# Optimization experiments

Hardware: AMD Instinct MI355X
Metric: run time of the kernel (lower is better)

## Reference

```python
import jax, jax.numpy as jnp
import numpy as np

K = 16          # top-k per pooled row
EPS = 1e-12     # tf.nn.l2_normalize epsilon


def setup_inputs() -> dict:
    key = jax.random.key(0)
    x = jax.random.normal(key, (16, 256, 128, 128), dtype=jnp.float32)
    return {"x": x}


def reference(x) -> tuple:
    # x: [B, C, H, W]; last_n_dims = 2 -> pool the trailing H*W axis.
    B, C, H, W = x.shape
    flat = x.reshape(B, C, H * W)                       # [B, C, HW]
    # tf.nn.l2_normalize(axis=-1): x / sqrt(max(sum(x^2), eps))
    sq = jnp.sum(flat * flat, axis=-1, keepdims=True)
    normed = flat * jax.lax.rsqrt(jnp.maximum(sq, EPS))  # [B, C, HW]
    top_k_value, top_k_idx = jax.lax.top_k(normed, K)    # [B, C, K]
    # decode flat indices into (h, w) coordinates (div/mod loop in original)
    h = top_k_idx // W
    w = top_k_idx % W
    coors = jnp.stack([h, w], axis=-1).astype(jnp.int32)  # [B, C, K, 2]
    return top_k_value, coors
```

## Files before the change

### kernel.cpp

```cpp
#include <hip/hip_runtime.h>


#define KSEL 16
#define HW   16384
#define QSZ  4096
#define WDIM 128
#define CAP  1024
#define CAPQ 256
#define T0   2.5f
#define NROWS 4096
#define NQ   (NROWS * 4)
#define VALS_TOTAL (NROWS * KSEL)

typedef float floatx4 __attribute__((ext_vector_type(4)));


__global__ __launch_bounds__(256) void k1_stream(const float* __restrict__ x,
                                                 float* __restrict__ qsum,
                                                 unsigned* __restrict__ qcnt,
                                                 unsigned long long* __restrict__ qcand) {
    const int b    = blockIdx.x;
    const int row  = b >> 2;
    const int q    = b & 3;
    const int t    = threadIdx.x;
    const int lane = t & 63;

    __shared__ unsigned long long s_cand[CAPQ];
    __shared__ unsigned s_cnt;
    __shared__ float s_part[4];

    if (t == 0) s_cnt = 0;
    __syncthreads();

    const floatx4* p = (const floatx4*)(x + (size_t)row * HW + q * QSZ);

    floatx4 buf[4];
    #pragma unroll
    for (int k = 0; k < 4; ++k)
        buf[k] = __builtin_nontemporal_load(&p[k * 256 + t]);

    float sumsq = 0.0f;
    #pragma unroll
    for (int k = 0; k < 4; ++k) {
        sumsq = fmaf(buf[k].x, buf[k].x, sumsq);
        sumsq = fmaf(buf[k].y, buf[k].y, sumsq);
        sumsq = fmaf(buf[k].z, buf[k].z, sumsq);
        sumsq = fmaf(buf[k].w, buf[k].w, sumsq);
    }

    unsigned msk = 0;
    #pragma unroll
    for (int k = 0; k < 4; ++k) {
        msk |= (buf[k].x > T0) ? (1u << (4 * k + 0)) : 0u;
        msk |= (buf[k].y > T0) ? (1u << (4 * k + 1)) : 0u;
        msk |= (buf[k].z > T0) ? (1u << (4 * k + 2)) : 0u;
        msk |= (buf[k].w > T0) ? (1u << (4 * k + 3)) : 0u;
    }
    unsigned base = 0;
    if (msk) base = atomicAdd(&s_cnt, (unsigned)__popc(msk));
    if (msk) {
        #pragma unroll
        for (int k = 0; k < 4; ++k) {
            #pragma unroll
            for (int c = 0; c < 4; ++c) {
                float v = (c == 0) ? buf[k].x : (c == 1) ? buf[k].y
                        : (c == 2) ? buf[k].z : buf[k].w;
                if (v > T0) {
                    if (base < CAPQ) {
                        unsigned u  = __float_as_uint(v);
                        unsigned mm = u ^ (((unsigned)((int)u >> 31)) | 0x80000000u);
                        int idx = q * QSZ + (k * 256 + t) * 4 + c;
                        s_cand[base] = ((unsigned long long)mm << 32) |
                                       (unsigned)(16383 - idx);
                    }
                    base++;
                }
            }
        }
    }

    #pragma unroll
    for (int off = 32; off > 0; off >>= 1)
        sumsq += __shfl_down(sumsq, off, 64);
    if (lane == 0) s_part[t >> 6] = sumsq;
    __syncthreads();

    unsigned cnt = s_cnt;
    unsigned wr = cnt < CAPQ ? cnt : CAPQ;
    for (unsigned i = t; i < wr; i += 256)
        qcand[(size_t)b * CAPQ + i] = s_cand[i];
    if (t == 0) {
        qcnt[b] = cnt;
        qsum[b] = s_part[0] + s_part[1] + s_part[2] + s_part[3];
    }
}

__global__ __launch_bounds__(256) void k2_select(const float* __restrict__ x,
                                                 const float* __restrict__ qsum,
                                                 const unsigned* __restrict__ qcnt,
                                                 const unsigned long long* __restrict__ qcand,
                                                 float* __restrict__ out) {
    const int row = blockIdx.x;
    const int t   = threadIdx.x;

    __shared__ unsigned long long s_cand[CAP];
    __shared__ unsigned s_qc[4];
    __shared__ float s_qs[4];
    __shared__ unsigned s_cnt;
    __shared__ float s_scale;

    if (t < 4) {
        s_qc[t] = qcnt[row * 4 + t];
        s_qs[t] = qsum[row * 4 + t];
    }
    __syncthreads();

    const unsigned c0 = s_qc[0], c1 = s_qc[1], c2 = s_qc[2], c3 = s_qc[3];
    if (t == 0)
        s_scale = 1.0f / sqrtf(fmaxf(s_qs[0] + s_qs[1] + s_qs[2] + s_qs[3], 1e-12f));
    const bool ovf = (c0 > CAPQ) | (c1 > CAPQ) | (c2 > CAPQ) | (c3 > CAPQ);
    const unsigned tot = c0 + c1 + c2 + c3;

    unsigned cnt;
    if (!ovf && tot >= KSEL && tot <= CAP) {
        const unsigned off[4] = {0u, c0, c0 + c1, c0 + c1 + c2};
        const unsigned cc[4]  = {c0, c1, c2, c3};
        #pragma unroll
        for (int q = 0; q < 4; ++q)
            for (unsigned i = t; i < cc[q]; i += 256)
                s_cand[off[q] + i] = qcand[(size_t)(row * 4 + q) * CAPQ + i];
        cnt = tot;
        __syncthreads();
    } else {
        const float* xr = x + (size_t)row * HW;
        float T = T0, lo = -3.0e38f, hi = 3.0e38f;
        cnt = 0;
        for (int it = 0; it < 32; ++it) {
            __syncthreads();
            if (t == 0) s_cnt = 0;
            __syncthreads();
            for (int i = t; i < HW; i += 256) {
                float v = xr[i];
                if (v > T) {
                    unsigned slot = atomicAdd(&s_cnt, 1u);
                    if (slot < CAP) {
                        unsigned u  = __float_as_uint(v);
                        unsigned mm = u ^ (((unsigned)((int)u >> 31)) | 0x80000000u);
                        s_cand[slot] = ((unsigned long long)mm << 32) |
                                       (unsigned)(16383 - i);
                    }
                }
            }
            __syncthreads();
            cnt = s_cnt;
            if (cnt >= KSEL && cnt <= CAP) break;
            if (cnt < KSEL) { hi = T; T = (lo < -1.0e38f) ? T - 1.0f : 0.5f * (lo + T); }
            else            { lo = T; T = (hi >  1.0e38f) ? T + 1.0f : 0.5f * (T + hi); }
        }
        if (cnt > CAP) cnt = CAP;
    }
    const float scale = s_scale;

    for (unsigned i = t; i < cnt; i += 256) {
        unsigned long long p = s_cand[i];
        unsigned m = (unsigned)(p >> 32);
        unsigned u = (m & 0x80000000u) ? (m ^ 0x80000000u) : ~m;
        float vn = __uint_as_float(u) * scale;
        unsigned u2 = __float_as_uint(vn);
        unsigned m2 = u2 ^ (((unsigned)((int)u2 >> 31)) | 0x80000000u);
        s_cand[i] = ((unsigned long long)m2 << 32) | (p & 0xFFFFFFFFull);
    }
    __syncthreads();

    for (unsigned i = t; i < cnt; i += 256) {
        unsigned long long p = s_cand[i];
        int rank = 0;
        for (unsigned j = 0; j < cnt; ++j) rank += (s_cand[j] > p) ? 1 : 0;
        if (rank < KSEL) {
            unsigned m = (unsigned)(p >> 32);
            unsigned u = (m & 0x80000000u) ? (m ^ 0x80000000u) : ~m;
            float vn = __uint_as_float(u);
            int idx = 16383 - (int)(unsigned)(p & 0xFFFFFFFFull);
            out[row * KSEL + rank] = vn;
            float* coor = out + VALS_TOTAL + ((size_t)row * KSEL + rank) * 2;
            coor[0] = (float)(idx >> 7);
            coor[1] = (float)(idx & (WDIM - 1));
        }
    }
}

extern "C" void kernel_launch(void* const* d_in, const int* in_sizes, int n_in,
                              void* d_out, int out_size, void* d_ws, size_t ws_size,
                              hipStream_t stream) {
    const float* x = (const float*)d_in[0];
    float* out = (float*)d_out;
    char* ws = (char*)d_ws;
    float* qsum = (float*)ws;
    unsigned* qcnt = (unsigned*)(ws + 64 * 1024);
    unsigned long long* qcand =
        (unsigned long long*)(ws + 128 * 1024);

    k1_stream<<<NQ, 256, 0, stream>>>(x, qsum, qcnt, qcand);
    k2_select<<<NROWS, 256, 0, stream>>>(x, qsum, qcnt, qcand, out);
}
```

Measured before the change: 343.2 us.

## Fuse streaming pass and selection into one kernel per row

Merges the quarter-row streaming kernel and the per-row selection kernel into a single kernel where each block streams a whole row in four chunks, gathering candidates above the threshold directly into a 1024-entry shared buffer. This removes the global round trip of candidates, counts and partial sums, and drops the second kernel launch. In exchange the grid shrinks from 16384 to 4096 blocks, each doing four times the streaming work and holding 8 KB of shared candidates, which may reduce memory-level parallelism.

```diff
diff --git a/kernel.cpp b/kernel.cpp
--- a/kernel.cpp
+++ b/kernel.cpp
@@ -3,138 +3,100 @@
 
 #define KSEL 16
 #define HW   16384
-#define QSZ  4096
 #define WDIM 128
 #define CAP  1024
-#define CAPQ 256
 #define T0   2.5f
 #define NROWS 4096
-#define NQ   (NROWS * 4)
 #define VALS_TOTAL (NROWS * KSEL)
 
 typedef float floatx4 __attribute__((ext_vector_type(4)));
 
-
-__global__ __launch_bounds__(256) void k1_stream(const float* __restrict__ x,
-                                                 float* __restrict__ qsum,
-                                                 unsigned* __restrict__ qcnt,
-                                                 unsigned long long* __restrict__ qcand) {
-    const int b    = blockIdx.x;
-    const int row  = b >> 2;
-    const int q    = b & 3;
+__global__ __launch_bounds__(256) void k_fused(const float* __restrict__ x,
+                                               float* __restrict__ out) {
+    const int row  = blockIdx.x;
     const int t    = threadIdx.x;
     const int lane = t & 63;
+    const int wv   = t >> 6;
 
-    __shared__ unsigned long long s_cand[CAPQ];
+    __shared__ unsigned long long s_cand[CAP];
+    __shared__ float s_part[4][4];
     __shared__ unsigned s_cnt;
-    __shared__ float s_part[4];
 
     if (t == 0) s_cnt = 0;
     __syncthreads();
 
-    const floatx4* p = (const floatx4*)(x + (size_t)row * HW + q * QSZ);
+    const floatx4* p = (const floatx4*)(x + (size_t)row * HW);
 
-    floatx4 buf[4];
+    float sqsum[4];
     #pragma unroll
-    for (int k = 0; k < 4; ++k)
-        buf[k] = __builtin_nontemporal_load(&p[k * 256 + t]);
+    for (int c = 0; c < 4; ++c) {
+        floatx4 buf[4];
+        #pragma unroll
+        for (int k = 0; k < 4; ++k)
+            buf[k] = __builtin_nontemporal_load(&p[c * 1024 + k * 256 + t]);
 
-    float sumsq = 0.0f;
-    #pragma unroll
-    for (int k = 0; k < 4; ++k) {
-        sumsq = fmaf(buf[k].x, buf[k].x, sumsq);
-        sumsq = fmaf(buf[k].y, buf[k].y, sumsq);
-        sumsq = fmaf(buf[k].z, buf[k].z, sumsq);
-        sumsq = fmaf(buf[k].w, buf[k].w, sumsq);
-    }
-
-    unsigned msk = 0;
-    #pragma unroll
-    for (int k = 0; k < 4; ++k) {
-        msk |= (buf[k].x > T0) ? (1u << (4 * k + 0)) : 0u;
-        msk |= (buf[k].y > T0) ? (1u << (4 * k + 1)) : 0u;
-        msk |= (buf[k].z > T0) ? (1u << (4 * k + 2)) : 0u;
-        msk |= (buf[k].w > T0) ? (1u << (4 * k + 3)) : 0u;
-    }
-    unsigned base = 0;
-    if (msk) base = atomicAdd(&s_cnt, (unsigned)__popc(msk));
-    if (msk) {
+        float s = 0.0f;
         #pragma unroll
         for (int k = 0; k < 4; ++k) {
+            s = fmaf(buf[k].x, buf[k].x, s);
+            s = fmaf(buf[k].y, buf[k].y, s);
+            s = fmaf(buf[k].z, buf[k].z, s);
+            s = fmaf(buf[k].w, buf[k].w, s);
+        }
+        sqsum[c] = s;
+
+        unsigned msk = 0;
+        #pragma unroll
+        for (int k = 0; k < 4; ++k) {
+            msk |= (buf[k].x > T0) ? (1u << (4 * k + 0)) : 0u;
+            msk |= (buf[k].y > T0) ? (1u << (4 * k + 1)) : 0u;
+            msk |= (buf[k].z > T0) ? (1u << (4 * k + 2)) : 0u;
+            msk |= (buf[k].w > T0) ? (1u << (4 * k + 3)) : 0u;
+        }
+        if (msk) {
+            unsigned base = atomicAdd(&s_cnt, (unsigned)__popc(msk));
             #pragma unroll
-            for (int c = 0; c < 4; ++c) {
-                float v = (c == 0) ? buf[k].x : (c == 1) ? buf[k].y
-                        : (c == 2) ? buf[k].z : buf[k].w;
-                if (v > T0) {
-                    if (base < CAPQ) {
-                        unsigned u  = __float_as_uint(v);
-                        unsigned mm = u ^ (((unsigned)((int)u >> 31)) | 0x80000000u);
-                        int idx = q * QSZ + (k * 256 + t) * 4 + c;
-                        s_cand[base] = ((unsigned long long)mm << 32) |
-                                       (unsigned)(16383 - idx);
+            for (int k = 0; k < 4; ++k) {
+                #pragma unroll
+                for (int cc = 0; cc < 4; ++cc) {
+                    float v = (cc == 0) ? buf[k].x : (cc == 1) ? buf[k].y
+                            : (cc == 2) ? buf[k].z : buf[k].w;
+                    if (v > T0) {
+                        if (base < CAP) {
+                            unsigned u  = __float_as_uint(v);
+                            unsigned mm = u ^ (((unsigned)((int)u >> 31)) | 0x80000000u);
+                            int idx = c * 4096 + (k * 256 + t) * 4 + cc;
+                            s_cand[base] = ((unsigned long long)mm << 32) |
+                                           (unsigned)(16383 - idx);
+                        }
+                        base++;
                     }
-                    base++;
                 }
             }
         }
     }
 
     #pragma unroll
-    for (int off = 32; off > 0; off >>= 1)
-        sumsq += __shfl_down(sumsq, off, 64);
-    if (lane == 0) s_part[t >> 6] = sumsq;
-    __syncthreads();
-
-    unsigned cnt = s_cnt;
-    unsigned wr = cnt < CAPQ ? cnt : CAPQ;
-    for (unsigned i = t; i < wr; i += 256)
-        qcand[(size_t)b * CAPQ + i] = s_cand[i];
-    if (t == 0) {
-        qcnt[b] = cnt;
-        qsum[b] = s_part[0] + s_part[1] + s_part[2] + s_part[3];
-    }
-}
-
-__global__ __launch_bounds__(256) void k2_select(const float* __restrict__ x,
-                                                 const float* __restrict__ qsum,
-                                                 const unsigned* __restrict__ qcnt,
-                                                 const unsigned long long* __restrict__ qcand,
-                                                 float* __restrict__ out) {
-    const int row = blockIdx.x;
-    const int t   = threadIdx.x;
-
-    __shared__ unsigned long long s_cand[CAP];
-    __shared__ unsigned s_qc[4];
-    __shared__ float s_qs[4];
-    __shared__ unsigned s_cnt;
-    __shared__ float s_scale;
-
-    if (t < 4) {
-        s_qc[t] = qcnt[row * 4 + t];
-        s_qs[t] = qsum[row * 4 + t];
+    for (int c = 0; c < 4; ++c) {
+        float s = sqsum[c];
+        #pragma unroll
+        for (int off = 32; off > 0; off >>= 1)
+            s += __shfl_down(s, off, 64);
+        if (lane == 0) s_part[c][wv] = s;
     }
     __syncthreads();
 
-    const unsigned c0 = s_qc[0], c1 = s_qc[1], c2 = s_qc[2], c3 = s_qc[3];
-    if (t == 0)
-        s_scale = 1.0f / sqrtf(fmaxf(s_qs[0] + s_qs[1] + s_qs[2] + s_qs[3], 1e-12f));
-    const bool ovf = (c0 > CAPQ) | (c1 > CAPQ) | (c2 > CAPQ) | (c3 > CAPQ);
-    const unsigned tot = c0 + c1 + c2 + c3;
+    const float q0 = s_part[0][0] + s_part[0][1] + s_part[0][2] + s_part[0][3];
+    const float q1 = s_part[1][0] + s_part[1][1] + s_part[1][2] + s_part[1][3];
+    const float q2 = s_part[2][0] + s_part[2][1] + s_part[2][2] + s_part[2][3];
+    const float q3 = s_part[3][0] + s_part[3][1] + s_part[3][2] + s_part[3][3];
+    const float scale = 1.0f / sqrtf(fmaxf(q0 + q1 + q2 + q3, 1e-12f));
 
-    unsigned cnt;
-    if (!ovf && tot >= KSEL && tot <= CAP) {
-        const unsigned off[4] = {0u, c0, c0 + c1, c0 + c1 + c2};
-        const unsigned cc[4]  = {c0, c1, c2, c3};
-        #pragma unroll
-        for (int q = 0; q < 4; ++q)
-            for (unsigned i = t; i < cc[q]; i += 256)
-                s_cand[off[q] + i] = qcand[(size_t)(row * 4 + q) * CAPQ + i];
-        cnt = tot;
-        __syncthreads();
-    } else {
+    unsigned cnt = s_cnt;
+
+    if (cnt < KSEL || cnt > CAP) {
         const float* xr = x + (size_t)row * HW;
         float T = T0, lo = -3.0e38f, hi = 3.0e38f;
-        cnt = 0;
         for (int it = 0; it < 32; ++it) {
             __syncthreads();
             if (t == 0) s_cnt = 0;
@@ -159,28 +121,27 @@
         }
         if (cnt > CAP) cnt = CAP;
     }
-    const float scale = s_scale;
 
     for (unsigned i = t; i < cnt; i += 256) {
-        unsigned long long p = s_cand[i];
-        unsigned m = (unsigned)(p >> 32);
+        unsigned long long pk = s_cand[i];
+        unsigned m = (unsigned)(pk >> 32);
         unsigned u = (m & 0x80000000u) ? (m ^ 0x80000000u) : ~m;
         float vn = __uint_as_float(u) * scale;
         unsigned u2 = __float_as_uint(vn);
         unsigned m2 = u2 ^ (((unsigned)((int)u2 >> 31)) | 0x80000000u);
-        s_cand[i] = ((unsigned long long)m2 << 32) | (p & 0xFFFFFFFFull);
+        s_cand[i] = ((unsigned long long)m2 << 32) | (pk & 0xFFFFFFFFull);
     }
     __syncthreads();
 
     for (unsigned i = t; i < cnt; i += 256) {
-        unsigned long long p = s_cand[i];
+        unsigned long long pk = s_cand[i];
         int rank = 0;
-        for (unsigned j = 0; j < cnt; ++j) rank += (s_cand[j] > p) ? 1 : 0;
+        for (unsigned j = 0; j < cnt; ++j) rank += (s_cand[j] > pk) ? 1 : 0;
         if (rank < KSEL) {
-            unsigned m = (unsigned)(p >> 32);
+            unsigned m = (unsigned)(pk >> 32);
             unsigned u = (m & 0x80000000u) ? (m ^ 0x80000000u) : ~m;
             float vn = __uint_as_float(u);
-            int idx = 16383 - (int)(unsigned)(p & 0xFFFFFFFFull);
+            int idx = 16383 - (int)(unsigned)(pk & 0xFFFFFFFFull);
             out[row * KSEL + rank] = vn;
             float* coor = out + VALS_TOTAL + ((size_t)row * KSEL + rank) * 2;
             coor[0] = (float)(idx >> 7);
@@ -194,12 +155,6 @@
                               hipStream_t stream) {
     const float* x = (const float*)d_in[0];
     float* out = (float*)d_out;
-    char* ws = (char*)d_ws;
-    float* qsum = (float*)ws;
-    unsigned* qcnt = (unsigned*)(ws + 64 * 1024);
-    unsigned long long* qcand =
-        (unsigned long long*)(ws + 128 * 1024);
-
-    k1_stream<<<NQ, 256, 0, stream>>>(x, qsum, qcnt, qcand);
-    k2_select<<<NROWS, 256, 0, stream>>>(x, qsum, qcnt, qcand, out);
+    (void)d_ws; (void)ws_size;
+    k_fused<<<NROWS, 256, 0, stream>>>(x, out);
 }
```

Result: faster. 330.7 us, median of 2 (-3.7%).
